# Performance work log

Hardware: AMD Instinct MI355X
Metric: run time of the kernel (lower is better)

Reference implementation:

```python
import jax, jax.numpy as jnp
import numpy as np

N_NODES = 50000


def _gine(x, src, dst, edge_embed, lin_w, lin_b, nn_w, nn_b):
    # PyG GINEConv (eps=0): out = nn(x + sum_{j->i} ReLU(x_j + lin(edge_attr)))
    e = edge_embed @ lin_w + lin_b              # [E, d_in]
    msg = jax.nn.relu(x[src] + e)               # gather + fuse, [E, d_in]
    agg = jax.ops.segment_sum(msg, dst, num_segments=N_NODES)  # scatter-add, [N, d_in]
    return (x + agg) @ nn_w + nn_b              # small MLP, [N, d_out]


def setup_inputs() -> dict:
    key = jax.random.key(0)
    ks = jax.random.split(key, 20)
    E = 800000
    h = 128
    sc = lambda f_in: 1.0 / np.sqrt(f_in)
    inp = {
        "x": jax.random.normal(ks[0], (N_NODES, 1), jnp.float32),
        "edge_index": jax.random.randint(ks[1], (2, E), 0, N_NODES, jnp.int64),
        "edge_attr": jax.random.normal(ks[2], (E, 1), jnp.float32),
        "em_w": jax.random.normal(ks[3], (1, h), jnp.float32) * sc(1),
        "em_b": jnp.zeros((h,), jnp.float32),
        "l1_w": jax.random.normal(ks[4], (h, 1), jnp.float32) * sc(h),
        "l1_b": jnp.zeros((1,), jnp.float32),
        "n1_w": jax.random.normal(ks[5], (1, h), jnp.float32) * sc(1),
        "n1_b": jnp.zeros((h,), jnp.float32),
        "l2_w": jax.random.normal(ks[6], (h, h), jnp.float32) * sc(h),
        "l2_b": jnp.zeros((h,), jnp.float32),
        "n2_w": jax.random.normal(ks[7], (h, h), jnp.float32) * sc(h),
        "n2_b": jnp.zeros((h,), jnp.float32),
        "l3_w": jax.random.normal(ks[8], (h, h), jnp.float32) * sc(h),
        "l3_b": jnp.zeros((h,), jnp.float32),
        "n3_w": jax.random.normal(ks[9], (h, h), jnp.float32) * sc(h),
        "n3_b": jnp.zeros((h,), jnp.float32),
        "dec_w": jax.random.normal(ks[10], (2 * h, 1), jnp.float32) * sc(2 * h),
        "dec_b": jnp.zeros((1,), jnp.float32),
    }
    return inp


def reference(x, edge_index, edge_attr, em_w, em_b, l1_w, l1_b, n1_w, n1_b,
              l2_w, l2_b, n2_w, n2_b, l3_w, l3_b, n3_w, n3_b, dec_w, dec_b):
    src, dst = edge_index[0], edge_index[1]
    edge_embed = edge_attr @ em_w + em_b                      # [E, 128]
    hdn = _gine(x,   src, dst, edge_embed, l1_w, l1_b, n1_w, n1_b)
    hdn = _gine(hdn, src, dst, edge_embed, l2_w, l2_b, n2_w, n2_b)
    hdn = _gine(hdn, src, dst, edge_embed, l3_w, l3_b, n3_w, n3_b)
    h_cat = jnp.concatenate([hdn[src], hdn[dst]], axis=-1)    # [E, 256]
    return h_cat @ dec_w + dec_b                              # [E, 1]
```

## Files before the change

kernel.cpp:

```cpp
#include <hip/hip_runtime.h>

#define H 128
#define CAPC 5376


typedef unsigned long long ull;
using bf16x8 = __attribute__((ext_vector_type(8))) short;
using f32x4  = __attribute__((ext_vector_type(4))) float;

__device__ __forceinline__ float bf2f(unsigned short v) {
  return __uint_as_float(((unsigned)v) << 16);
}
__device__ __forceinline__ unsigned short bf16r(float v) {
  unsigned u = __float_as_uint(v);
  u = (u + 0x7FFFu + ((u >> 16) & 1u)) >> 16;
  return (unsigned short)u;
}
__device__ __forceinline__ unsigned bf16pair(float a, float b) {
  return (unsigned)bf16r(a) | ((unsigned)bf16r(b) << 16);
}

__global__ __launch_bounds__(256) void init_consts(
    const float* __restrict__ em_w, const float* __restrict__ em_b,
    const float* __restrict__ l1_w, const float* __restrict__ l1_b,
    const float* __restrict__ l2_w, const float* __restrict__ l2_b,
    const float* __restrict__ n1_b,
    const float* __restrict__ l3_w, const float* __restrict__ l3_b,
    const float* __restrict__ n2w, const float* __restrict__ n3w,
    float* __restrict__ consts, int* __restrict__ cursor,
    unsigned short* __restrict__ w2t, unsigned short* __restrict__ w3t,
    int NBUCK) {
  if (blockIdx.x > 0) {
    const int i = (blockIdx.x - 1) * 256 + threadIdx.x;
    if (i < H * H) {
      const int j = i >> 7, k = i & (H - 1);
      w2t[k * H + j] = bf16r(n2w[i]);
    } else {
      const int ii = i - H * H;
      const int j = ii >> 7, k = ii & (H - 1);
      w3t[k * H + j] = bf16r(n3w[ii]);
    }
    return;
  }
  const int k = threadIdx.x;
  if (k < NBUCK) cursor[k] = 0;
  __shared__ float sa[H], sc[H];
  if (k < H) {
    float u2 = 0.f, c2 = 0.f, u3 = 0.f, c3 = 0.f;
    for (int j = 0; j < H; ++j) {
      const float ew = em_w[j], eb = em_b[j];
      u2 = fmaf(ew, l2_w[j * H + k], u2);
      c2 = fmaf(eb, l2_w[j * H + k], c2);
      u3 = fmaf(ew, l3_w[j * H + k], u3);
      c3 = fmaf(eb, l3_w[j * H + k], c3);
    }
    consts[2 + k]         = u2;
    consts[2 + H + k]     = c2 + l2_b[k] + n1_b[k];
    consts[2 + 2 * H + k] = u3;
    consts[2 + 3 * H + k] = c3 + l3_b[k];
    sa[k] = em_w[k] * l1_w[k];
    sc[k] = em_b[k] * l1_w[k];
  }
  __syncthreads();
  for (int s = 64; s > 0; s >>= 1) {
    if (k < s) { sa[k] += sa[k + s]; sc[k] += sc[k + s]; }
    __syncthreads();
  }
  if (k == 0) { consts[0] = sa[0]; consts[1] = sc[0] + l1_b[0]; }
}

__global__ __launch_bounds__(1024) void bin_scatter(
    const int* __restrict__ src, const int* __restrict__ dst,
    const float* __restrict__ ea, int* __restrict__ cursor,
    ull* __restrict__ spc, int E, int NBUCK) {
  __shared__ int lhist[256];
  __shared__ int lbase[256];
  const int tid = threadIdx.x;
  const int base = blockIdx.x * 2048 + tid * 2;
  if (tid < 256) lhist[tid] = 0;
  __syncthreads();
  int s_[2], d_[2], b_[2], r_[2];
  float a_[2];
#pragma unroll
  for (int j = 0; j < 2; ++j) {
    const int e = base + j;
    if (e < E) {
      s_[j] = src[e]; d_[j] = dst[e]; a_[j] = ea[e];
      b_[j] = d_[j] >> 8;
      r_[j] = atomicAdd(&lhist[b_[j]], 1);
    } else {
      b_[j] = -1;
    }
  }
  __syncthreads();
  if (tid < NBUCK && lhist[tid] > 0)
    lbase[tid] = atomicAdd(&cursor[tid], lhist[tid]);
  __syncthreads();
#pragma unroll
  for (int j = 0; j < 2; ++j) {
    if (b_[j] >= 0) {
      const int pl = lbase[b_[j]] + r_[j];
      if (pl < CAPC)
        spc[(size_t)b_[j] * CAPC + pl] =
            ((ull)(unsigned)(s_[j] | ((d_[j] & 255) << 16)) << 32) |
            (ull)(unsigned)__float_as_uint(a_[j]);
    }
  }
}

__global__ __launch_bounds__(1024) void fine_scatter(
    const int* __restrict__ cursor, const ull* __restrict__ spc,
    const float* __restrict__ x, const float* __restrict__ consts,
    int2* __restrict__ spf, int* __restrict__ rowstart,
    float* __restrict__ s1, int N) {
  __shared__ int lh[256];
  __shared__ int sd[256];
  __shared__ int cur[256];
  __shared__ int2 pay[CAPC];
  const int tid = threadIdx.x;
  const int b = blockIdx.x;
  const int cnt = min(cursor[b], CAPC);
  const size_t rbase = (size_t)b * CAPC;
  if (tid < 256) lh[tid] = 0;
  __syncthreads();
  for (int i = tid; i < cnt; i += 1024)
    atomicAdd(&lh[(int)((spc[rbase + i] >> 48) & 255u)], 1);
  __syncthreads();
  if (tid < 256) sd[tid] = lh[tid];
  __syncthreads();
  for (int off = 1; off < 256; off <<= 1) {
    int t = 0;
    if (tid < 256 && tid >= off) t = sd[tid - off];
    __syncthreads();
    if (tid < 256) sd[tid] += t;
    __syncthreads();
  }
  if (tid < 256) {
    const int ex = sd[tid] - lh[tid];
    cur[tid] = ex;
    rowstart[b * 257 + tid] = (int)rbase + ex;
    if (tid == 0) rowstart[b * 257 + 256] = (int)rbase + cnt;
  }
  __syncthreads();
  for (int i = tid; i < cnt; i += 1024) {
    const ull payv = spc[rbase + i];
    const int dl = (int)((payv >> 48) & 255u);
    const int pos = atomicAdd(&cur[dl], 1);
    pay[pos] = make_int2((int)((payv >> 32) & 0xFFFFu), (int)(unsigned)payv);
  }
  __syncthreads();
  for (int i = tid; i < cnt; i += 1024) spf[rbase + i] = pay[i];
  const int lane = tid & 63, wid = tid >> 6;
  const float a1 = consts[0], c1 = consts[1];
  for (int i = wid; i < 256; i += 16) {
    const int n = (b << 8) + i;
    if (n >= N) break;
    const int rsl = sd[i] - lh[i], ci = lh[i];
    float part = 0.f;
    for (int j = lane; j < ci; j += 64) {
      const int2 pv = pay[rsl + j];
      part += fmaxf(x[pv.x] + fmaf(a1, __int_as_float(pv.y), c1), 0.f);
    }
#pragma unroll
    for (int o = 32; o >= 1; o >>= 1) part += __shfl_xor(part, o, 64);
    if (lane == 0) s1[n] = x[n] + part;
  }
}

__global__ __launch_bounds__(256) void edge2_csr(
    const int* __restrict__ rowstart, const int2* __restrict__ sp,
    const float* __restrict__ s1, const float* __restrict__ n1w,
    const float* __restrict__ n1b, const float* __restrict__ consts,
    unsigned short* __restrict__ t2b, int N) {
  const int n = (blockIdx.x * blockDim.x + threadIdx.x) >> 6;
  const int lane = threadIdx.x & 63;
  if (n >= N) return;
  const int rbase = (n >> 8) * 257 + (n & 255);
  const int rs = rowstart[rbase], re = rowstart[rbase + 1];
  const float w0 = n1w[lane],            w1 = n1w[lane + 64];
  const float u0 = consts[2 + lane],     u1 = consts[2 + lane + 64];
  const float c0 = consts[2 + H + lane], c1 = consts[2 + H + lane + 64];
  float acc0 = 0.f, acc1 = 0.f;
  for (int base = rs; base < re; base += 64) {
    const int i = base + lane;
    float s1v = 0.f, eav = 0.f;
    if (i < re) {
      const int2 sv = sp[i];
      s1v = s1[sv.x];
      eav = __int_as_float(sv.y);
    }
    const int cnt = min(64, re - base);
    for (int j = 0; j < cnt; ++j) {
      const float s = __shfl(s1v, j, 64);
      const float a = __shfl(eav, j, 64);
      acc0 += fmaxf(fmaf(s, w0, fmaf(a, u0, c0)), 0.f);
      acc1 += fmaxf(fmaf(s, w1, fmaf(a, u1, c1)), 0.f);
    }
  }
  const float sn = s1[n];
  t2b[(size_t)n * H + lane]      = bf16r(fmaf(sn, w0, n1b[lane])      + acc0);
  t2b[(size_t)n * H + lane + 64] = bf16r(fmaf(sn, w1, n1b[lane + 64]) + acc1);
}

__global__ __launch_bounds__(256) void edge3_csr(
    const int* __restrict__ rowstart, const int2* __restrict__ sp,
    const unsigned short* __restrict__ h2b, const float* __restrict__ consts,
    unsigned short* __restrict__ t3b, int N) {
  const int n = (blockIdx.x * blockDim.x + threadIdx.x) >> 6;
  const int lane = threadIdx.x & 63;
  if (n >= N) return;
  const int rbase = (n >> 8) * 257 + (n & 255);
  const int rs = rowstart[rbase], re = rowstart[rbase + 1];
  const int k0 = 2 * lane;
  const float u0 = consts[2 + 2 * H + k0], u1 = consts[2 + 2 * H + k0 + 1];
  const float c0 = consts[2 + 3 * H + k0], c1 = consts[2 + 3 * H + k0 + 1];
  float acc0 = 0.f, acc1 = 0.f;
  int i = rs;
  for (; i + 4 <= re; i += 4) {
    const int2 e0 = sp[i], e1 = sp[i + 1], e2 = sp[i + 2], e3 = sp[i + 3];
    const ushort2 h0 = *(const ushort2*)&h2b[(size_t)e0.x * H + k0];
    const ushort2 h1 = *(const ushort2*)&h2b[(size_t)e1.x * H + k0];
    const ushort2 h2v = *(const ushort2*)&h2b[(size_t)e2.x * H + k0];
    const ushort2 h3 = *(const ushort2*)&h2b[(size_t)e3.x * H + k0];
    const float a0 = __int_as_float(e0.y), a1 = __int_as_float(e1.y);
    const float a2 = __int_as_float(e2.y), a3 = __int_as_float(e3.y);
    acc0 += fmaxf(bf2f(h0.x) + fmaf(a0, u0, c0), 0.f);
    acc1 += fmaxf(bf2f(h0.y) + fmaf(a0, u1, c1), 0.f);
    acc0 += fmaxf(bf2f(h1.x) + fmaf(a1, u0, c0), 0.f);
    acc1 += fmaxf(bf2f(h1.y) + fmaf(a1, u1, c1), 0.f);
    acc0 += fmaxf(bf2f(h2v.x) + fmaf(a2, u0, c0), 0.f);
    acc1 += fmaxf(bf2f(h2v.y) + fmaf(a2, u1, c1), 0.f);
    acc0 += fmaxf(bf2f(h3.x) + fmaf(a3, u0, c0), 0.f);
    acc1 += fmaxf(bf2f(h3.y) + fmaf(a3, u1, c1), 0.f);
  }
  for (; i < re; ++i) {
    const int2 ev = sp[i];
    const ushort2 hv = *(const ushort2*)&h2b[(size_t)ev.x * H + k0];
    const float a = __int_as_float(ev.y);
    acc0 += fmaxf(bf2f(hv.x) + fmaf(a, u0, c0), 0.f);
    acc1 += fmaxf(bf2f(hv.y) + fmaf(a, u1, c1), 0.f);
  }
  const ushort2 hn = *(const ushort2*)&h2b[(size_t)n * H + k0];
  ((unsigned*)t3b)[(size_t)n * 64 + lane] =
      bf16pair(bf2f(hn.x) + acc0, bf2f(hn.y) + acc1);
}

__global__ __launch_bounds__(256) void mlp2_mfma(
    const unsigned short* __restrict__ t2b, unsigned short* __restrict__ h2b,
    const unsigned short* __restrict__ w2t, const float* __restrict__ n2b,
    int N) {
  __shared__ unsigned short dt[4][16 * H];
  const int tid = threadIdx.x, w = tid >> 6, lane = tid & 63;
  const int col = lane & 15, quad = lane >> 4;
  const int tile = blockIdx.x * 4 + w;
  const int node0 = tile * 16;
  const bf16x8* arow =
      (const bf16x8*)(t2b + (size_t)(node0 + col) * H + quad * 8);
  const bf16x8 a0 = arow[0], a1 = arow[4], a2 = arow[8], a3 = arow[12];
#pragma unroll
  for (int t = 0; t < 8; ++t) {
    const bf16x8* bcol =
        (const bf16x8*)(w2t + (size_t)(t * 16 + col) * H + quad * 8);
    f32x4 acc = {0.f, 0.f, 0.f, 0.f};
    acc = __builtin_amdgcn_mfma_f32_16x16x32_bf16(a0, bcol[0], acc, 0, 0, 0);
    acc = __builtin_amdgcn_mfma_f32_16x16x32_bf16(a1, bcol[4], acc, 0, 0, 0);
    acc = __builtin_amdgcn_mfma_f32_16x16x32_bf16(a2, bcol[8], acc, 0, 0, 0);
    acc = __builtin_amdgcn_mfma_f32_16x16x32_bf16(a3, bcol[12], acc, 0, 0, 0);
    const float bias = n2b[t * 16 + col];
#pragma unroll
    for (int r = 0; r < 4; ++r)
      dt[w][(quad * 4 + r) * H + t * 16 + col] = bf16r(acc[r] + bias);
  }
  __syncthreads();
  const unsigned* du = (const unsigned*)dt;
  unsigned* gu = (unsigned*)h2b;
  const int nb = blockIdx.x * 64;
  for (int i = tid; i < 64 * 64; i += 256) {
    const int r = i >> 6;
    if (nb + r < N) gu[(size_t)(nb + r) * 64 + (i & 63)] = du[i];
  }
}

__global__ __launch_bounds__(256) void mlp3_mfma(
    const unsigned short* __restrict__ t3b, const unsigned short* __restrict__ w3t,
    const float* __restrict__ n3b, const float* __restrict__ dec_w,
    float* __restrict__ p, float* __restrict__ q, int N) {
  __shared__ float dt3[4][16 * H];
  const int tid = threadIdx.x, w = tid >> 6, lane = tid & 63;
  const int col = lane & 15, quad = lane >> 4;
  const int tile = blockIdx.x * 4 + w;
  const int node0 = tile * 16;
  const bf16x8* arow =
      (const bf16x8*)(t3b + (size_t)(node0 + col) * H + quad * 8);
  const bf16x8 a0 = arow[0], a1 = arow[4], a2 = arow[8], a3 = arow[12];
#pragma unroll
  for (int t = 0; t < 8; ++t) {
    const bf16x8* bcol =
        (const bf16x8*)(w3t + (size_t)(t * 16 + col) * H + quad * 8);
    f32x4 acc = {0.f, 0.f, 0.f, 0.f};
    acc = __builtin_amdgcn_mfma_f32_16x16x32_bf16(a0, bcol[0], acc, 0, 0, 0);
    acc = __builtin_amdgcn_mfma_f32_16x16x32_bf16(a1, bcol[4], acc, 0, 0, 0);
    acc = __builtin_amdgcn_mfma_f32_16x16x32_bf16(a2, bcol[8], acc, 0, 0, 0);
    acc = __builtin_amdgcn_mfma_f32_16x16x32_bf16(a3, bcol[12], acc, 0, 0, 0);
    const float bias = n3b[t * 16 + col];
#pragma unroll
    for (int r = 0; r < 4; ++r)
      dt3[w][(quad * 4 + r) * H + t * 16 + col] = acc[r] + bias;
  }
  __syncthreads();
  const float dwA0 = dec_w[lane], dwA1 = dec_w[64 + lane];
  const float dwB0 = dec_w[128 + lane], dwB1 = dec_w[192 + lane];
#pragma unroll 4
  for (int r = 0; r < 16; ++r) {
    const float h0 = dt3[w][r * H + lane];
    const float h1 = dt3[w][r * H + 64 + lane];
    float pd = h0 * dwA0 + h1 * dwA1;
    float qd = h0 * dwB0 + h1 * dwB1;
#pragma unroll
    for (int o = 32; o >= 1; o >>= 1) {
      pd += __shfl_xor(pd, o, 64);
      qd += __shfl_xor(qd, o, 64);
    }
    const int n = node0 + r;
    if (lane == 0 && n < N) { p[n] = pd; q[n] = qd; }
  }
}

__global__ void final_kernel(const int* __restrict__ src,
                             const int* __restrict__ dst,
                             const float* __restrict__ p,
                             const float* __restrict__ q,
                             const float* __restrict__ dec_b,
                             float* __restrict__ out, int E) {
  const int e = blockIdx.x * blockDim.x + threadIdx.x;
  if (e < E) out[e] = p[src[e]] + q[dst[e]] + dec_b[0];
}

extern "C" void kernel_launch(void* const* d_in, const int* in_sizes, int n_in,
                              void* d_out, int out_size, void* d_ws, size_t ws_size,
                              hipStream_t stream) {
  const float* x     = (const float*)d_in[0];
  const int*   ei    = (const int*)d_in[1];
  const float* ea    = (const float*)d_in[2];
  const float* em_w  = (const float*)d_in[3];
  const float* em_b  = (const float*)d_in[4];
  const float* l1_w  = (const float*)d_in[5];
  const float* l1_b  = (const float*)d_in[6];
  const float* n1_w  = (const float*)d_in[7];
  const float* n1_b  = (const float*)d_in[8];
  const float* l2_w  = (const float*)d_in[9];
  const float* l2_b  = (const float*)d_in[10];
  const float* n2_w  = (const float*)d_in[11];
  const float* n2_b  = (const float*)d_in[12];
  const float* l3_w  = (const float*)d_in[13];
  const float* l3_b  = (const float*)d_in[14];
  const float* n3_w  = (const float*)d_in[15];
  const float* n3_b  = (const float*)d_in[16];
  const float* dec_w = (const float*)d_in[17];
  const float* dec_b = (const float*)d_in[18];
  float* out = (float*)d_out;

  const int N = in_sizes[0];
  const int E = in_sizes[2];
  const int* src = ei;
  const int* dst = ei + E;

  const int NBUCK  = (N + 255) >> 8;
  const int NBATCH = (E + 2047) >> 11;
  const int NPAD   = ((N + 63) / 64) * 64;
  const int NBLK64 = NPAD / 64;

  float* ws       = (float*)d_ws;
  float* consts   = ws;
  ull*   spc      = (ull*)(ws + 1024);
  int2*  spf      = (int2*)(spc + (size_t)NBUCK * CAPC);
  unsigned short* t2b = (unsigned short*)(spf + (size_t)NBUCK * CAPC);
  unsigned short* t3b = t2b + (size_t)NPAD * H;
  unsigned short* h2b = t3b + (size_t)NPAD * H;
  unsigned short* w2t = h2b + (size_t)NPAD * H;
  unsigned short* w3t = w2t + H * H;
  float* s1       = (float*)(w3t + H * H);
  float* p        = s1 + N;
  float* q        = p + N;
  int*   cursor   = (int*)(q + N);
  int*   rowstart = cursor + 256;

  init_consts<<<129, 256, 0, stream>>>(em_w, em_b, l1_w, l1_b, l2_w, l2_b,
                                       n1_b, l3_w, l3_b, n2_w, n3_w,
                                       consts, cursor, w2t, w3t, NBUCK);
  bin_scatter<<<NBATCH, 1024, 0, stream>>>(src, dst, ea, cursor, spc, E, NBUCK);
  fine_scatter<<<NBUCK, 1024, 0, stream>>>(cursor, spc, x, consts, spf,
                                           rowstart, s1, N);

  const int nwblocks = (N + 3) / 4;
  edge2_csr<<<nwblocks, 256, 0, stream>>>(rowstart, spf, s1, n1_w, n1_b,
                                          consts, t2b, N);
  mlp2_mfma<<<NBLK64, 256, 0, stream>>>(t2b, h2b, w2t, n2_b, N);
  edge3_csr<<<nwblocks, 256, 0, stream>>>(rowstart, spf, h2b, consts, t3b, N);
  mlp3_mfma<<<NBLK64, 256, 0, stream>>>(t3b, w3t, n3_b, dec_w, p, q, N);
  final_kernel<<<(E + 255) / 256, 256, 0, stream>>>(src, dst, p, q, dec_b, out, E);
}
```

Before: 246.7 us.

## Fuse edge aggregation with MFMA MLP per layer and use 128-node buckets

Merges each layer's CSR edge aggregation and its bf16 MFMA MLP into one 1024-thread kernel. Each wave aggregates one of 16 nodes into shared memory, then eight waves run the 16x128x128 MFMA. This removes the t2b/t3b global round trips and two launches. Bucket granularity also drops from 256 to 128 nodes per bucket with a smaller per-bucket capacity, which shrinks fine_scatter's shared memory so more blocks can run at once. The smaller capacity raises the risk of silently dropping edges when a bucket overflows, and only 16 nodes per block gives a small MFMA phase with idle waves.

```diff
diff --git a/kernel.cpp b/kernel.cpp
--- a/kernel.cpp
+++ b/kernel.cpp
@@ -1,7 +1,7 @@
 #include <hip/hip_runtime.h>
 
 #define H 128
-#define CAPC 5376
+#define CAPC 3072
 
 
 typedef unsigned long long ull;
@@ -28,8 +28,7 @@
     const float* __restrict__ l3_w, const float* __restrict__ l3_b,
     const float* __restrict__ n2w, const float* __restrict__ n3w,
     float* __restrict__ consts, int* __restrict__ cursor,
-    unsigned short* __restrict__ w2t, unsigned short* __restrict__ w3t,
-    int NBUCK) {
+    unsigned short* __restrict__ w2t, unsigned short* __restrict__ w3t) {
   if (blockIdx.x > 0) {
     const int i = (blockIdx.x - 1) * 256 + threadIdx.x;
     if (i < H * H) {
@@ -43,7 +42,8 @@
     return;
   }
   const int k = threadIdx.x;
-  if (k < NBUCK) cursor[k] = 0;
+  cursor[k] = 0;
+  cursor[k + 256] = 0;
   __shared__ float sa[H], sc[H];
   if (k < H) {
     float u2 = 0.f, c2 = 0.f, u3 = 0.f, c3 = 0.f;
@@ -73,11 +73,11 @@
     const int* __restrict__ src, const int* __restrict__ dst,
     const float* __restrict__ ea, int* __restrict__ cursor,
     ull* __restrict__ spc, int E, int NBUCK) {
-  __shared__ int lhist[256];
-  __shared__ int lbase[256];
+  __shared__ int lhist[512];
+  __shared__ int lbase[512];
   const int tid = threadIdx.x;
   const int base = blockIdx.x * 2048 + tid * 2;
-  if (tid < 256) lhist[tid] = 0;
+  if (tid < 512) lhist[tid] = 0;
   __syncthreads();
   int s_[2], d_[2], b_[2], r_[2];
   float a_[2];
@@ -86,7 +86,7 @@
     const int e = base + j;
     if (e < E) {
       s_[j] = src[e]; d_[j] = dst[e]; a_[j] = ea[e];
-      b_[j] = d_[j] >> 8;
+      b_[j] = d_[j] >> 7;
       r_[j] = atomicAdd(&lhist[b_[j]], 1);
     } else {
       b_[j] = -1;
@@ -102,7 +102,7 @@
       const int pl = lbase[b_[j]] + r_[j];
       if (pl < CAPC)
         spc[(size_t)b_[j] * CAPC + pl] =
-            ((ull)(unsigned)(s_[j] | ((d_[j] & 255) << 16)) << 32) |
+            ((ull)(unsigned)(s_[j] | ((d_[j] & 127) << 16)) << 32) |
             (ull)(unsigned)__float_as_uint(a_[j]);
     }
   }
@@ -113,47 +113,47 @@
     const float* __restrict__ x, const float* __restrict__ consts,
     int2* __restrict__ spf, int* __restrict__ rowstart,
     float* __restrict__ s1, int N) {
-  __shared__ int lh[256];
-  __shared__ int sd[256];
-  __shared__ int cur[256];
+  __shared__ int lh[128];
+  __shared__ int sd[128];
+  __shared__ int cur[128];
   __shared__ int2 pay[CAPC];
   const int tid = threadIdx.x;
   const int b = blockIdx.x;
   const int cnt = min(cursor[b], CAPC);
   const size_t rbase = (size_t)b * CAPC;
-  if (tid < 256) lh[tid] = 0;
+  if (tid < 128) lh[tid] = 0;
   __syncthreads();
   for (int i = tid; i < cnt; i += 1024)
-    atomicAdd(&lh[(int)((spc[rbase + i] >> 48) & 255u)], 1);
-  __syncthreads();
-  if (tid < 256) sd[tid] = lh[tid];
-  __syncthreads();
-  for (int off = 1; off < 256; off <<= 1) {
+    atomicAdd(&lh[(int)((spc[rbase + i] >> 48) & 127u)], 1);
+  __syncthreads();
+  if (tid < 128) sd[tid] = lh[tid];
+  __syncthreads();
+  for (int off = 1; off < 128; off <<= 1) {
     int t = 0;
-    if (tid < 256 && tid >= off) t = sd[tid - off];
+    if (tid < 128 && tid >= off) t = sd[tid - off];
     __syncthreads();
-    if (tid < 256) sd[tid] += t;
+    if (tid < 128) sd[tid] += t;
     __syncthreads();
   }
-  if (tid < 256) {
+  if (tid < 128) {
     const int ex = sd[tid] - lh[tid];
     cur[tid] = ex;
-    rowstart[b * 257 + tid] = (int)rbase + ex;
-    if (tid == 0) rowstart[b * 257 + 256] = (int)rbase + cnt;
+    rowstart[b * 129 + tid] = (int)rbase + ex;
+    if (tid == 0) rowstart[b * 129 + 128] = (int)rbase + cnt;
   }
   __syncthreads();
   for (int i = tid; i < cnt; i += 1024) {
     const ull payv = spc[rbase + i];
-    const int dl = (int)((payv >> 48) & 255u);
+    const int dl = (int)((payv >> 48) & 127u);
     const int pos = atomicAdd(&cur[dl], 1);
     pay[pos] = make_int2((int)((payv >> 32) & 0xFFFFu), (int)(unsigned)payv);
   }
   __syncthreads();
   for (int i = tid; i < cnt; i += 1024) spf[rbase + i] = pay[i];
-  const int lane = tid & 63, wid = tid >> 6;
+  const int lane = tid & 63, w = tid >> 6;
   const float a1 = consts[0], c1 = consts[1];
-  for (int i = wid; i < 256; i += 16) {
-    const int n = (b << 8) + i;
+  for (int i = w; i < 128; i += 16) {
+    const int n = (b << 7) + i;
     if (n >= N) break;
     const int rsl = sd[i] - lh[i], ci = lh[i];
     float part = 0.f;
@@ -167,98 +167,56 @@
   }
 }
 
-__global__ __launch_bounds__(256) void edge2_csr(
+__global__ __launch_bounds__(1024) void layer2_fused(
     const int* __restrict__ rowstart, const int2* __restrict__ sp,
     const float* __restrict__ s1, const float* __restrict__ n1w,
     const float* __restrict__ n1b, const float* __restrict__ consts,
-    unsigned short* __restrict__ t2b, int N) {
-  const int n = (blockIdx.x * blockDim.x + threadIdx.x) >> 6;
-  const int lane = threadIdx.x & 63;
-  if (n >= N) return;
-  const int rbase = (n >> 8) * 257 + (n & 255);
-  const int rs = rowstart[rbase], re = rowstart[rbase + 1];
-  const float w0 = n1w[lane],            w1 = n1w[lane + 64];
-  const float u0 = consts[2 + lane],     u1 = consts[2 + lane + 64];
-  const float c0 = consts[2 + H + lane], c1 = consts[2 + H + lane + 64];
-  float acc0 = 0.f, acc1 = 0.f;
-  for (int base = rs; base < re; base += 64) {
-    const int i = base + lane;
-    float s1v = 0.f, eav = 0.f;
-    if (i < re) {
-      const int2 sv = sp[i];
-      s1v = s1[sv.x];
-      eav = __int_as_float(sv.y);
-    }
-    const int cnt = min(64, re - base);
-    for (int j = 0; j < cnt; ++j) {
-      const float s = __shfl(s1v, j, 64);
-      const float a = __shfl(eav, j, 64);
-      acc0 += fmaxf(fmaf(s, w0, fmaf(a, u0, c0)), 0.f);
-      acc1 += fmaxf(fmaf(s, w1, fmaf(a, u1, c1)), 0.f);
-    }
-  }
-  const float sn = s1[n];
-  t2b[(size_t)n * H + lane]      = bf16r(fmaf(sn, w0, n1b[lane])      + acc0);
-  t2b[(size_t)n * H + lane + 64] = bf16r(fmaf(sn, w1, n1b[lane + 64]) + acc1);
-}
-
-__global__ __launch_bounds__(256) void edge3_csr(
-    const int* __restrict__ rowstart, const int2* __restrict__ sp,
-    const unsigned short* __restrict__ h2b, const float* __restrict__ consts,
-    unsigned short* __restrict__ t3b, int N) {
-  const int n = (blockIdx.x * blockDim.x + threadIdx.x) >> 6;
-  const int lane = threadIdx.x & 63;
-  if (n >= N) return;
-  const int rbase = (n >> 8) * 257 + (n & 255);
-  const int rs = rowstart[rbase], re = rowstart[rbase + 1];
-  const int k0 = 2 * lane;
-  const float u0 = consts[2 + 2 * H + k0], u1 = consts[2 + 2 * H + k0 + 1];
-  const float c0 = consts[2 + 3 * H + k0], c1 = consts[2 + 3 * H + k0 + 1];
-  float acc0 = 0.f, acc1 = 0.f;
-  int i = rs;
-  for (; i + 4 <= re; i += 4) {
-    const int2 e0 = sp[i], e1 = sp[i + 1], e2 = sp[i + 2], e3 = sp[i + 3];
-    const ushort2 h0 = *(const ushort2*)&h2b[(size_t)e0.x * H + k0];
-    const ushort2 h1 = *(const ushort2*)&h2b[(size_t)e1.x * H + k0];
-    const ushort2 h2v = *(const ushort2*)&h2b[(size_t)e2.x * H + k0];
-    const ushort2 h3 = *(const ushort2*)&h2b[(size_t)e3.x * H + k0];
-    const float a0 = __int_as_float(e0.y), a1 = __int_as_float(e1.y);
-    const float a2 = __int_as_float(e2.y), a3 = __int_as_float(e3.y);
-    acc0 += fmaxf(bf2f(h0.x) + fmaf(a0, u0, c0), 0.f);
-    acc1 += fmaxf(bf2f(h0.y) + fmaf(a0, u1, c1), 0.f);
-    acc0 += fmaxf(bf2f(h1.x) + fmaf(a1, u0, c0), 0.f);
-    acc1 += fmaxf(bf2f(h1.y) + fmaf(a1, u1, c1), 0.f);
-    acc0 += fmaxf(bf2f(h2v.x) + fmaf(a2, u0, c0), 0.f);
-    acc1 += fmaxf(bf2f(h2v.y) + fmaf(a2, u1, c1), 0.f);
-    acc0 += fmaxf(bf2f(h3.x) + fmaf(a3, u0, c0), 0.f);
-    acc1 += fmaxf(bf2f(h3.y) + fmaf(a3, u1, c1), 0.f);
-  }
-  for (; i < re; ++i) {
-    const int2 ev = sp[i];
-    const ushort2 hv = *(const ushort2*)&h2b[(size_t)ev.x * H + k0];
-    const float a = __int_as_float(ev.y);
-    acc0 += fmaxf(bf2f(hv.x) + fmaf(a, u0, c0), 0.f);
-    acc1 += fmaxf(bf2f(hv.y) + fmaf(a, u1, c1), 0.f);
-  }
-  const ushort2 hn = *(const ushort2*)&h2b[(size_t)n * H + k0];
-  ((unsigned*)t3b)[(size_t)n * 64 + lane] =
-      bf16pair(bf2f(hn.x) + acc0, bf2f(hn.y) + acc1);
-}
-
-__global__ __launch_bounds__(256) void mlp2_mfma(
-    const unsigned short* __restrict__ t2b, unsigned short* __restrict__ h2b,
     const unsigned short* __restrict__ w2t, const float* __restrict__ n2b,
-    int N) {
-  __shared__ unsigned short dt[4][16 * H];
+    unsigned short* __restrict__ h2b, int N) {
+  __shared__ unsigned short t2s[16][136];
+  __shared__ unsigned short hs[16][128];
   const int tid = threadIdx.x, w = tid >> 6, lane = tid & 63;
-  const int col = lane & 15, quad = lane >> 4;
-  const int tile = blockIdx.x * 4 + w;
-  const int node0 = tile * 16;
-  const bf16x8* arow =
-      (const bf16x8*)(t2b + (size_t)(node0 + col) * H + quad * 8);
-  const bf16x8 a0 = arow[0], a1 = arow[4], a2 = arow[8], a3 = arow[12];
-#pragma unroll
-  for (int t = 0; t < 8; ++t) {
+  const int node0 = blockIdx.x * 16;
+  {
+    const int n = node0 + w;
+    if (n < N) {
+      const int rb = (n >> 7) * 129 + (n & 127);
+      const int rs = rowstart[rb], re = rowstart[rb + 1];
+      const float w0 = n1w[lane],            w1 = n1w[lane + 64];
+      const float u0 = consts[2 + lane],     u1 = consts[2 + lane + 64];
+      const float c0 = consts[2 + H + lane], c1 = consts[2 + H + lane + 64];
+      float acc0 = 0.f, acc1 = 0.f;
+      for (int base = rs; base < re; base += 64) {
+        const int i = base + lane;
+        float s1v = 0.f, eav = 0.f;
+        if (i < re) {
+          const int2 sv = sp[i];
+          s1v = s1[sv.x];
+          eav = __int_as_float(sv.y);
+        }
+        const int cntv = min(64, re - base);
+        for (int j = 0; j < cntv; ++j) {
+          const float s = __shfl(s1v, j, 64);
+          const float a = __shfl(eav, j, 64);
+          acc0 += fmaxf(fmaf(s, w0, fmaf(a, u0, c0)), 0.f);
+          acc1 += fmaxf(fmaf(s, w1, fmaf(a, u1, c1)), 0.f);
+        }
+      }
+      const float sn = s1[n];
+      t2s[w][lane]      = bf16r(fmaf(sn, w0, n1b[lane])      + acc0);
+      t2s[w][lane + 64] = bf16r(fmaf(sn, w1, n1b[lane + 64]) + acc1);
+    } else {
+      t2s[w][lane] = 0;
+      t2s[w][lane + 64] = 0;
+    }
+  }
+  __syncthreads();
+  if (w < 8) {
+    const int t = w, col = lane & 15, quad = lane >> 4;
+    const bf16x8 a0 = *(const bf16x8*)&t2s[col][quad * 8];
+    const bf16x8 a1 = *(const bf16x8*)&t2s[col][32 + quad * 8];
+    const bf16x8 a2 = *(const bf16x8*)&t2s[col][64 + quad * 8];
+    const bf16x8 a3 = *(const bf16x8*)&t2s[col][96 + quad * 8];
     const bf16x8* bcol =
         (const bf16x8*)(w2t + (size_t)(t * 16 + col) * H + quad * 8);
     f32x4 acc = {0.f, 0.f, 0.f, 0.f};
@@ -269,32 +227,72 @@
     const float bias = n2b[t * 16 + col];
 #pragma unroll
     for (int r = 0; r < 4; ++r)
-      dt[w][(quad * 4 + r) * H + t * 16 + col] = bf16r(acc[r] + bias);
-  }
-  __syncthreads();
-  const unsigned* du = (const unsigned*)dt;
-  unsigned* gu = (unsigned*)h2b;
-  const int nb = blockIdx.x * 64;
-  for (int i = tid; i < 64 * 64; i += 256) {
-    const int r = i >> 6;
-    if (nb + r < N) gu[(size_t)(nb + r) * 64 + (i & 63)] = du[i];
-  }
-}
-
-__global__ __launch_bounds__(256) void mlp3_mfma(
-    const unsigned short* __restrict__ t3b, const unsigned short* __restrict__ w3t,
-    const float* __restrict__ n3b, const float* __restrict__ dec_w,
-    float* __restrict__ p, float* __restrict__ q, int N) {
-  __shared__ float dt3[4][16 * H];
+      hs[quad * 4 + r][t * 16 + col] = bf16r(acc[r] + bias);
+  }
+  __syncthreads();
+  const int row = tid >> 6, word = tid & 63;
+  ((unsigned*)h2b)[(size_t)(node0 + row) * 64 + word] =
+      ((const unsigned*)hs)[row * 64 + word];
+}
+
+__global__ __launch_bounds__(1024) void layer3_fused(
+    const int* __restrict__ rowstart, const int2* __restrict__ sp,
+    const unsigned short* __restrict__ h2b, const float* __restrict__ consts,
+    const unsigned short* __restrict__ w3t, const float* __restrict__ n3b,
+    const float* __restrict__ dec_w, float* __restrict__ p,
+    float* __restrict__ q, int N) {
+  __shared__ unsigned short t3s[16][136];
+  __shared__ float ps[16], qs[16];
   const int tid = threadIdx.x, w = tid >> 6, lane = tid & 63;
-  const int col = lane & 15, quad = lane >> 4;
-  const int tile = blockIdx.x * 4 + w;
-  const int node0 = tile * 16;
-  const bf16x8* arow =
-      (const bf16x8*)(t3b + (size_t)(node0 + col) * H + quad * 8);
-  const bf16x8 a0 = arow[0], a1 = arow[4], a2 = arow[8], a3 = arow[12];
-#pragma unroll
-  for (int t = 0; t < 8; ++t) {
+  const int node0 = blockIdx.x * 16;
+  if (tid < 16) { ps[tid] = 0.f; qs[tid] = 0.f; }
+  {
+    const int n = node0 + w;
+    const int k0 = 2 * lane;
+    if (n < N) {
+      const int rb = (n >> 7) * 129 + (n & 127);
+      const int rs = rowstart[rb], re = rowstart[rb + 1];
+      const float u0 = consts[2 + 2 * H + k0], u1 = consts[2 + 2 * H + k0 + 1];
+      const float c0 = consts[2 + 3 * H + k0], c1 = consts[2 + 3 * H + k0 + 1];
+      float acc0 = 0.f, acc1 = 0.f;
+      int i = rs;
+      for (; i + 4 <= re; i += 4) {
+        const int2 e0 = sp[i], e1 = sp[i + 1], e2 = sp[i + 2], e3 = sp[i + 3];
+        const ushort2 h0 = *(const ushort2*)&h2b[(size_t)e0.x * H + k0];
+        const ushort2 h1 = *(const ushort2*)&h2b[(size_t)e1.x * H + k0];
+        const ushort2 h2v = *(const ushort2*)&h2b[(size_t)e2.x * H + k0];
+        const ushort2 h3 = *(const ushort2*)&h2b[(size_t)e3.x * H + k0];
+        const float a0 = __int_as_float(e0.y), a1 = __int_as_float(e1.y);
+        const float a2 = __int_as_float(e2.y), a3 = __int_as_float(e3.y);
+        acc0 += fmaxf(bf2f(h0.x) + fmaf(a0, u0, c0), 0.f);
+        acc1 += fmaxf(bf2f(h0.y) + fmaf(a0, u1, c1), 0.f);
+        acc0 += fmaxf(bf2f(h1.x) + fmaf(a1, u0, c0), 0.f);
+        acc1 += fmaxf(bf2f(h1.y) + fmaf(a1, u1, c1), 0.f);
+        acc0 += fmaxf(bf2f(h2v.x) + fmaf(a2, u0, c0), 0.f);
+        acc1 += fmaxf(bf2f(h2v.y) + fmaf(a2, u1, c1), 0.f);
+        acc0 += fmaxf(bf2f(h3.x) + fmaf(a3, u0, c0), 0.f);
+        acc1 += fmaxf(bf2f(h3.y) + fmaf(a3, u1, c1), 0.f);
+      }
+      for (; i < re; ++i) {
+        const int2 ev = sp[i];
+        const ushort2 hv = *(const ushort2*)&h2b[(size_t)ev.x * H + k0];
+        const float a = __int_as_float(ev.y);
+        acc0 += fmaxf(bf2f(hv.x) + fmaf(a, u0, c0), 0.f);
+        acc1 += fmaxf(bf2f(hv.y) + fmaf(a, u1, c1), 0.f);
+      }
+      const ushort2 hn = *(const ushort2*)&h2b[(size_t)n * H + k0];
+      *(unsigned*)&t3s[w][k0] = bf16pair(bf2f(hn.x) + acc0, bf2f(hn.y) + acc1);
+    } else {
+      *(unsigned*)&t3s[w][k0] = 0u;
+    }
+  }
+  __syncthreads();
+  if (w < 8) {
+    const int t = w, col = lane & 15, quad = lane >> 4;
+    const bf16x8 a0 = *(const bf16x8*)&t3s[col][quad * 8];
+    const bf16x8 a1 = *(const bf16x8*)&t3s[col][32 + quad * 8];
+    const bf16x8 a2 = *(const bf16x8*)&t3s[col][64 + quad * 8];
+    const bf16x8 a3 = *(const bf16x8*)&t3s[col][96 + quad * 8];
     const bf16x8* bcol =
         (const bf16x8*)(w3t + (size_t)(t * 16 + col) * H + quad * 8);
     f32x4 acc = {0.f, 0.f, 0.f, 0.f};
@@ -303,26 +301,35 @@
     acc = __builtin_amdgcn_mfma_f32_16x16x32_bf16(a2, bcol[8], acc, 0, 0, 0);
     acc = __builtin_amdgcn_mfma_f32_16x16x32_bf16(a3, bcol[12], acc, 0, 0, 0);
     const float bias = n3b[t * 16 + col];
-#pragma unroll
-    for (int r = 0; r < 4; ++r)
-      dt3[w][(quad * 4 + r) * H + t * 16 + col] = acc[r] + bias;
-  }
-  __syncthreads();
-  const float dwA0 = dec_w[lane], dwA1 = dec_w[64 + lane];
-  const float dwB0 = dec_w[128 + lane], dwB1 = dec_w[192 + lane];
-#pragma unroll 4
-  for (int r = 0; r < 16; ++r) {
-    const float h0 = dt3[w][r * H + lane];
-    const float h1 = dt3[w][r * H + 64 + lane];
-    float pd = h0 * dwA0 + h1 * dwA1;
-    float qd = h0 * dwB0 + h1 * dwB1;
-#pragma unroll
-    for (int o = 32; o >= 1; o >>= 1) {
-      pd += __shfl_xor(pd, o, 64);
-      qd += __shfl_xor(qd, o, 64);
-    }
-    const int n = node0 + r;
-    if (lane == 0 && n < N) { p[n] = pd; q[n] = qd; }
+    const float dA = dec_w[t * 16 + col];
+    const float dB = dec_w[128 + t * 16 + col];
+    float pP[4], qP[4];
+#pragma unroll
+    for (int r = 0; r < 4; ++r) {
+      const float h = acc[r] + bias;
+      pP[r] = h * dA;
+      qP[r] = h * dB;
+    }
+#pragma unroll
+    for (int o = 1; o < 16; o <<= 1) {
+#pragma unroll
+      for (int r = 0; r < 4; ++r) {
+        pP[r] += __shfl_xor(pP[r], o, 64);
+        qP[r] += __shfl_xor(qP[r], o, 64);
+      }
+    }
+    if (col == 0) {
+#pragma unroll
+      for (int r = 0; r < 4; ++r) {
+        atomicAdd(&ps[quad * 4 + r], pP[r]);
+        atomicAdd(&qs[quad * 4 + r], qP[r]);
+      }
+    }
+  }
+  __syncthreads();
+  if (tid < 16) {
+    const int n = node0 + tid;
+    if (n < N) { p[n] = ps[tid]; q[n] = qs[tid]; }
   }
 }
 
@@ -365,38 +372,33 @@
   const int* src = ei;
   const int* dst = ei + E;
 
-  const int NBUCK  = (N + 255) >> 8;
+  const int NBUCK  = (N + 127) >> 7;
   const int NBATCH = (E + 2047) >> 11;
-  const int NPAD   = ((N + 63) / 64) * 64;
-  const int NBLK64 = NPAD / 64;
+  const int NPAD   = ((N + 15) / 16) * 16;
+  const int NT16   = NPAD / 16;
 
   float* ws       = (float*)d_ws;
   float* consts   = ws;
   ull*   spc      = (ull*)(ws + 1024);
   int2*  spf      = (int2*)(spc + (size_t)NBUCK * CAPC);
-  unsigned short* t2b = (unsigned short*)(spf + (size_t)NBUCK * CAPC);
-  unsigned short* t3b = t2b + (size_t)NPAD * H;
-  unsigned short* h2b = t3b + (size_t)NPAD * H;
+  unsigned short* h2b = (unsigned short*)(spf + (size_t)NBUCK * CAPC);
   unsigned short* w2t = h2b + (size_t)NPAD * H;
   unsigned short* w3t = w2t + H * H;
   float* s1       = (float*)(w3t + H * H);
   float* p        = s1 + N;
   float* q        = p + N;
   int*   cursor   = (int*)(q + N);
-  int*   rowstart = cursor + 256;
+  int*   rowstart = cursor + 512;
 
   init_consts<<<129, 256, 0, stream>>>(em_w, em_b, l1_w, l1_b, l2_w, l2_b,
                                        n1_b, l3_w, l3_b, n2_w, n3_w,
-                                       consts, cursor, w2t, w3t, NBUCK);
+                                       consts, cursor, w2t, w3t);
   bin_scatter<<<NBATCH, 1024, 0, stream>>>(src, dst, ea, cursor, spc, E, NBUCK);
   fine_scatter<<<NBUCK, 1024, 0, stream>>>(cursor, spc, x, consts, spf,
                                            rowstart, s1, N);
-
-  const int nwblocks = (N + 3) / 4;
-  edge2_csr<<<nwblocks, 256, 0, stream>>>(rowstart, spf, s1, n1_w, n1_b,
-                                          consts, t2b, N);
-  mlp2_mfma<<<NBLK64, 256, 0, stream>>>(t2b, h2b, w2t, n2_b, N);
-  edge3_csr<<<nwblocks, 256, 0, stream>>>(rowstart, spf, h2b, consts, t3b, N);
-  mlp3_mfma<<<NBLK64, 256, 0, stream>>>(t3b, w3t, n3_b, dec_w, p, q, N);
+  layer2_fused<<<NT16, 1024, 0, stream>>>(rowstart, spf, s1, n1_w, n1_b,
+                                          consts, w2t, n2_b, h2b, N);
+  layer3_fused<<<NT16, 1024, 0, stream>>>(rowstart, spf, h2b, consts, w3t,
+                                          n3_b, dec_w, p, q, N);
   final_kernel<<<(E + 255) / 256, 256, 0, stream>>>(src, dst, p, q, dec_b, out, E);
 }
```

Measured after the change: 236.9 us. -4.0%, faster.
